# Optimization experiments

Hardware: AMD Instinct MI355X
Metric: run time of the kernel (lower is better)

The kernel has to match this reference:

```python
import jax, jax.numpy as jnp
import numpy as np

B, N, C, H, S = 8, 1024, 768, 8, 16  # C = 3 * S * S, head_dim = C // H
NCH = 3
D = C // H
SCALE = D ** -0.5
REATTEN_SCALE = 1.0  # transform_scale=False
EPS = 1e-5  # BatchNorm2d eps


def conv3x3(x, w, b):
    # x: (B*N, 3, S, S); w: (O=3, I=3, 3, 3) OIHW; 'same' padding
    y = jax.lax.conv_general_dilated(x, w, (1, 1), 'SAME',
                                     dimension_numbers=('NCHW', 'OIHW', 'NCHW'))
    return y + b[None, :, None, None]


def setup_inputs() -> dict:
    key = jax.random.key(0)
    ks = jax.random.split(key, 8)
    return {
        'x': jax.random.normal(ks[0], (B, N, C), jnp.float32),
        'qw': jax.random.normal(ks[1], (NCH, NCH, 3, 3), jnp.float32) * 0.1,
        'qb': jnp.zeros((NCH,), jnp.float32),
        'kw': jax.random.normal(ks[2], (NCH, NCH, 3, 3), jnp.float32) * 0.1,
        'kb': jnp.zeros((NCH,), jnp.float32),
        'vw': jax.random.normal(ks[3], (NCH, NCH, 3, 3), jnp.float32) * 0.1,
        'vb': jnp.zeros((NCH,), jnp.float32),
        'rw': jax.random.normal(ks[4], (H, H), jnp.float32) * 0.2,  # 1x1 conv over heads
        'rb': jnp.zeros((H,), jnp.float32),
        'bn_g': jnp.ones((H,), jnp.float32),
        'bn_b': jnp.zeros((H,), jnp.float32),
        'bn_m': jnp.zeros((H,), jnp.float32),   # running mean
        'bn_v': jnp.ones((H,), jnp.float32),    # running var
        'pw': jax.random.normal(ks[5], (C, C), jnp.float32) * 0.02,
        'pb': jnp.zeros((C,), jnp.float32),
    }


def reference(x, qw, qb, kw, kb, vw, vb, rw, rb, bn_g, bn_b, bn_m, bn_v, pw, pb):
    Bx, Nx, Cx = x.shape
    xs = x.reshape(Bx * Nx, NCH, S, S)  # unflatten; all (b, n) convs batched at once

    def heads(y):  # (B*N, 3, S, S) -> (B, H, N, D)
        return y.reshape(Bx, Nx, H, D).transpose(0, 2, 1, 3)

    q = heads(conv3x3(xs, qw, qb))
    k = heads(conv3x3(xs, kw, kb))
    v = heads(conv3x3(xs, vw, vb))

    attn = jnp.einsum('bhnd,bhmd->bhnm', q, k) * SCALE  # (B, H, N, N)
    attn = jax.nn.softmax(attn, axis=-1)
    # re-attention: 1x1 conv across heads, then BatchNorm2d (eval, running stats)
    attn = jnp.einsum('oh,bhnm->bonm', rw, attn) + rb[None, :, None, None]
    inv = (bn_g / jnp.sqrt(bn_v + EPS))[None, :, None, None]
    attn = (attn - bn_m[None, :, None, None]) * inv + bn_b[None, :, None, None]
    attn = attn * REATTEN_SCALE

    out = jnp.einsum('bhnm,bhmd->bhnd', attn, v)  # (B, H, N, D)
    out = out.transpose(0, 2, 1, 3).reshape(Bx, Nx, Cx)
    out = out @ pw.T + pb
    return (out, attn)
```

## Files before the change

kernel.cpp:

```cpp
#include <hip/hip_runtime.h>
#include <math.h>

#define B_ 8
#define N_ 1024
#define C_ 768
#define H_ 8
#define D_ 96
#define SCALE_F 0.1020620726159657f

typedef unsigned short u16;
typedef __bf16 bf16x8 __attribute__((ext_vector_type(8)));
typedef float f32x4 __attribute__((ext_vector_type(4)));

#define MFMA(a, b, c) __builtin_amdgcn_mfma_f32_16x16x32_bf16(a, b, c, 0, 0, 0)

__device__ inline void split1(float x, u16& h, u16& l) {
    __bf16 hb = (__bf16)x;
    float hf = (float)hb;
    __bf16 lb = (__bf16)(x - hf);
    h = __builtin_bit_cast(u16, hb);
    l = __builtin_bit_cast(u16, lb);
}

__device__ inline void split4(float4 x, ushort4& h, ushort4& l) {
    split1(x.x, h.x, l.x);
    split1(x.y, h.y, l.y);
    split1(x.z, h.z, l.z);
    split1(x.w, h.w, l.w);
}

__global__ __launch_bounds__(256) void conv_qkv(
    const float* __restrict__ x,
    const float* __restrict__ qw, const float* __restrict__ qb,
    const float* __restrict__ kw, const float* __restrict__ kb,
    const float* __restrict__ vw, const float* __restrict__ vb,
    u16* __restrict__ qh, u16* __restrict__ ql,
    u16* __restrict__ kh, u16* __restrict__ kl,
    float* __restrict__ v)
{
    __shared__ float simg[768];
    __shared__ float sw[243];
    __shared__ float sb[9];
    const int img = blockIdx.x;
    const int b = img >> 10;
    const int tid = threadIdx.x;

    for (int i = tid; i < 768; i += 256) simg[i] = x[(size_t)img * 768 + i];
    if (tid < 243) {
        int g = tid / 81, i = tid % 81;
        const float* w = (g == 0) ? qw : (g == 1) ? kw : vw;
        sw[tid] = w[i];
    }
    if (tid < 9) {
        int g = tid / 3, i = tid % 3;
        const float* bb = (g == 0) ? qb : (g == 1) ? kb : vb;
        sb[tid] = bb[i];
    }
    __syncthreads();

    const int n = img & 1023;
    for (int e = tid; e < 2304; e += 256) {
        int g = e / 768, c = e % 768;
        int oc = c >> 8, rem = c & 255, y = rem >> 4, xx = rem & 15;
        float acc = sb[g * 3 + oc];
        const float* wg = &sw[g * 81 + oc * 27];
        #pragma unroll
        for (int ic = 0; ic < 3; ++ic)
            #pragma unroll
            for (int ky = 0; ky < 3; ++ky) {
                int yy = y + ky - 1;
                if (yy < 0 || yy > 15) continue;
                #pragma unroll
                for (int kx = 0; kx < 3; ++kx) {
                    int xp = xx + kx - 1;
                    if (xp < 0 || xp > 15) continue;
                    acc += wg[ic * 9 + ky * 3 + kx] * simg[ic * 256 + yy * 16 + xp];
                }
            }
        int hh = c / 96, d = c % 96;
        size_t o = ((size_t)(b * 8 + hh) * 1024 + n) * 96 + d;
        if (g == 2) {
            v[o] = acc;
        } else {
            u16 hi, lo;
            split1(acc, hi, lo);
            if (g == 0) { qh[o] = hi; ql[o] = lo; }
            else        { kh[o] = hi; kl[o] = lo; }
        }
    }
}

__global__ __launch_bounds__(256) void vt_split(
    const float* __restrict__ v, u16* __restrict__ vt_h)
{
    __shared__ float t32[32][36];
    const int bh = blockIdx.z, n0 = blockIdx.x * 32, d0 = blockIdx.y * 32;
    const int tid = threadIdx.x;
    {
        int nn = tid >> 3, c4 = (tid & 7) * 4;
        float4 x = *(const float4*)&v[((size_t)bh * 1024 + n0 + nn) * 96 + d0 + c4];
        t32[nn][c4] = x.x; t32[nn][c4 + 1] = x.y;
        t32[nn][c4 + 2] = x.z; t32[nn][c4 + 3] = x.w;
    }
    __syncthreads();
    {
        int d = tid >> 3, n4 = (tid & 7) * 4;
        ushort4 h;
        h.x = __builtin_bit_cast(u16, (__bf16)t32[n4][d]);
        h.y = __builtin_bit_cast(u16, (__bf16)t32[n4 + 1][d]);
        h.z = __builtin_bit_cast(u16, (__bf16)t32[n4 + 2][d]);
        h.w = __builtin_bit_cast(u16, (__bf16)t32[n4 + 3][d]);
        size_t o = ((size_t)bh * 96 + d0 + d) * 1024 + n0 + n4;
        *(ushort4*)&vt_h[o] = h;
    }
}

__global__ __launch_bounds__(256) void pw_split(
    const float* __restrict__ pw, u16* __restrict__ pwh, u16* __restrict__ pwl)
{
    int i = blockIdx.x * 256 + threadIdx.x;
    float4 x = *(const float4*)&pw[(size_t)i * 4];
    ushort4 h, l;
    split4(x, h, l);
    *(ushort4*)&pwh[(size_t)i * 4] = h;
    *(ushort4*)&pwl[(size_t)i * 4] = l;
}

__global__ __launch_bounds__(512) void fused_attn(
    const u16* __restrict__ qh, const u16* __restrict__ ql,
    const u16* __restrict__ kh, const u16* __restrict__ kl,
    const u16* __restrict__ vth,
    const float* __restrict__ rw, const float* __restrict__ rb,
    const float* __restrict__ bn_g, const float* __restrict__ bn_b,
    const float* __restrict__ bn_m, const float* __restrict__ bn_v,
    float* __restrict__ attn, u16* __restrict__ o1h, u16* __restrict__ o1l)
{
    __shared__ float p_lds[2][8][32][36];
    __shared__ float s_w2[8][8];
    __shared__ float s_b2[8];

    const int bid = blockIdx.x;
    const int b = bid & 7;
    const int n0 = (bid >> 3) * 32;
    const int tid = threadIdx.x, wid = tid >> 6, lane = tid & 63;
    const int l16 = lane & 15, kg = lane >> 4;
    const int h = wid;
    const size_t bh = (size_t)(b * 8 + h);

    if (tid < 64) {
        int o = tid >> 3, hh = tid & 7;
        float inv = bn_g[o] * rsqrtf(bn_v[o] + 1e-5f);
        s_w2[o][hh] = rw[o * 8 + hh] * inv;
        if (hh == 0) s_b2[o] = (rb[o] - bn_m[o]) * inv + bn_b[o];
    }

    bf16x8 qhf[2][3], qlf[2][3];
    #pragma unroll
    for (int nf = 0; nf < 2; ++nf)
        #pragma unroll
        for (int ks = 0; ks < 3; ++ks) {
            size_t off = (bh * 1024 + n0 + nf * 16 + l16) * 96 + ks * 32 + kg * 8;
            qhf[nf][ks] = *(const bf16x8*)&qh[off];
            qlf[nf][ks] = *(const bf16x8*)&ql[off];
        }

    float ls[2][4];
    #pragma unroll
    for (int nf = 0; nf < 2; ++nf)
        #pragma unroll
        for (int r = 0; r < 4; ++r) ls[nf][r] = 0.f;

    #pragma unroll 1
    for (int mt = 0; mt < 16; ++mt) {
        const int m0 = mt * 64;
        f32x4 sacc[2][4];
        #pragma unroll
        for (int nf = 0; nf < 2; ++nf)
            #pragma unroll
            for (int mf = 0; mf < 4; ++mf) sacc[nf][mf] = (f32x4){0.f, 0.f, 0.f, 0.f};

        __builtin_amdgcn_s_setprio(1);
        #pragma unroll
        for (int ks = 0; ks < 3; ++ks) {
            bf16x8 kbh[4];
            #pragma unroll
            for (int mf = 0; mf < 4; ++mf) {
                size_t off = (bh * 1024 + m0 + mf * 16 + l16) * 96 + ks * 32 + kg * 8;
                kbh[mf] = *(const bf16x8*)&kh[off];
            }
            #pragma unroll
            for (int nf = 0; nf < 2; ++nf)
                #pragma unroll
                for (int mf = 0; mf < 4; ++mf)
                    sacc[nf][mf] = MFMA(qhf[nf][ks], kbh[mf], sacc[nf][mf]);
        }
        __builtin_amdgcn_s_setprio(0);

        #pragma unroll
        for (int nf = 0; nf < 2; ++nf)
            #pragma unroll
            for (int mf = 0; mf < 4; ++mf)
                #pragma unroll
                for (int r = 0; r < 4; ++r)
                    ls[nf][r] += __expf(sacc[nf][mf][r] * SCALE_F);
    }

    float rv[2][4];
    #pragma unroll
    for (int nf = 0; nf < 2; ++nf)
        #pragma unroll
        for (int r = 0; r < 4; ++r) {
            float s = ls[nf][r];
            #pragma unroll
            for (int off = 1; off < 16; off <<= 1) s += __shfl_xor(s, off);
            rv[nf][r] = 1.0f / s;
        }

    __syncthreads();

    float w2r[8];
    #pragma unroll
    for (int hh = 0; hh < 8; ++hh) w2r[hh] = s_w2[h][hh];
    const float b2h = s_b2[h];

    f32x4 pvacc[2][6];
    #pragma unroll
    for (int nf = 0; nf < 2; ++nf)
        #pragma unroll
        for (int df = 0; df < 6; ++df) pvacc[nf][df] = (f32x4){0.f, 0.f, 0.f, 0.f};

    #pragma unroll 1
    for (int mt = 0; mt < 32; ++mt) {
        const int m0 = mt * 32;
        const int buf = mt & 1;

        bf16x8 vbh[6];
        #pragma unroll
        for (int df = 0; df < 6; ++df) {
            size_t off = (bh * 96 + df * 16 + l16) * 1024 + m0 + kg * 8;
            vbh[df] = *(const bf16x8*)&vth[off];
        }

        f32x4 sacc[2][2];
        #pragma unroll
        for (int nf = 0; nf < 2; ++nf)
            #pragma unroll
            for (int mf = 0; mf < 2; ++mf) sacc[nf][mf] = (f32x4){0.f, 0.f, 0.f, 0.f};
        __builtin_amdgcn_s_setprio(1);
        #pragma unroll
        for (int ks = 0; ks < 3; ++ks) {
            bf16x8 kbh[2], kbl[2];
            #pragma unroll
            for (int mf = 0; mf < 2; ++mf) {
                size_t off = (bh * 1024 + m0 + mf * 16 + l16) * 96 + ks * 32 + kg * 8;
                kbh[mf] = *(const bf16x8*)&kh[off];
                kbl[mf] = *(const bf16x8*)&kl[off];
            }
            #pragma unroll
            for (int nf = 0; nf < 2; ++nf)
                #pragma unroll
                for (int mf = 0; mf < 2; ++mf) {
                    sacc[nf][mf] = MFMA(qhf[nf][ks], kbh[mf], sacc[nf][mf]);
                    sacc[nf][mf] = MFMA(qhf[nf][ks], kbl[mf], sacc[nf][mf]);
                    sacc[nf][mf] = MFMA(qlf[nf][ks], kbh[mf], sacc[nf][mf]);
                }
        }
        __builtin_amdgcn_s_setprio(0);

        #pragma unroll
        for (int nf = 0; nf < 2; ++nf)
            #pragma unroll
            for (int mf = 0; mf < 2; ++mf)
                #pragma unroll
                for (int r = 0; r < 4; ++r) {
                    float pp = __expf(sacc[nf][mf][r] * SCALE_F) * rv[nf][r];
                    p_lds[buf][h][nf * 16 + kg * 4 + r][mf * 16 + l16] = pp;
                }
        __syncthreads();

        float mixf[2][8];
        #pragma unroll
        for (int nf = 0; nf < 2; ++nf)
            #pragma unroll
            for (int j = 0; j < 8; ++j) mixf[nf][j] = b2h;
        #pragma unroll
        for (int hh = 0; hh < 8; ++hh) {
            float w = w2r[hh];
            #pragma unroll
            for (int nf = 0; nf < 2; ++nf) {
                const float* pp = &p_lds[buf][hh][nf * 16 + l16][kg * 8];
                float4 a0 = *(const float4*)pp;
                float4 a1 = *(const float4*)(pp + 4);
                mixf[nf][0] += w * a0.x; mixf[nf][1] += w * a0.y;
                mixf[nf][2] += w * a0.z; mixf[nf][3] += w * a0.w;
                mixf[nf][4] += w * a1.x; mixf[nf][5] += w * a1.y;
                mixf[nf][6] += w * a1.z; mixf[nf][7] += w * a1.w;
            }
        }

        #pragma unroll
        for (int nf = 0; nf < 2; ++nf) {
            float* gp = &attn[(bh * 1024 + n0 + nf * 16 + l16) * 1024 + m0 + kg * 8];
            f32x4 v0 = {mixf[nf][0], mixf[nf][1], mixf[nf][2], mixf[nf][3]};
            f32x4 v1 = {mixf[nf][4], mixf[nf][5], mixf[nf][6], mixf[nf][7]};
            __builtin_nontemporal_store(v0, (f32x4*)gp);
            __builtin_nontemporal_store(v1, (f32x4*)(gp + 4));
        }

        bf16x8 mah[2];
        #pragma unroll
        for (int nf = 0; nf < 2; ++nf)
            #pragma unroll
            for (int j = 0; j < 8; ++j)
                mah[nf][j] = (__bf16)mixf[nf][j];
        __builtin_amdgcn_s_setprio(1);
        #pragma unroll
        for (int df = 0; df < 6; ++df)
            #pragma unroll
            for (int nf = 0; nf < 2; ++nf)
                pvacc[nf][df] = MFMA(mah[nf], vbh[df], pvacc[nf][df]);
        __builtin_amdgcn_s_setprio(0);
    }

    #pragma unroll
    for (int nf = 0; nf < 2; ++nf)
        #pragma unroll
        for (int df = 0; df < 6; ++df)
            #pragma unroll
            for (int r = 0; r < 4; ++r) {
                int row = n0 + nf * 16 + kg * 4 + r;
                int col = h * 96 + df * 16 + l16;
                u16 hh2, ll2;
                split1(pvacc[nf][df][r], hh2, ll2);
                size_t o = ((size_t)b * 1024 + row) * 768 + col;
                o1h[o] = hh2;
                o1l[o] = ll2;
            }
}

__global__ __launch_bounds__(256) void proj_mfma(
    const u16* __restrict__ o1h, const u16* __restrict__ o1l,
    const u16* __restrict__ pwh, const u16* __restrict__ pwl,
    const float* __restrict__ pb, float* __restrict__ out)
{
    __shared__ __align__(16) u16 Ahs[5120], Als[5120];
    __shared__ __align__(16) u16 Bhs[2560], Bls[2560];
    const int t0 = blockIdx.y * 128, o0 = blockIdx.x * 64;
    const int tid = threadIdx.x;
    const int wid = tid >> 6, lane = tid & 63;
    const int l16 = lane & 15, kg = lane >> 4;
    const int wr = wid >> 1, wc = wid & 1;

    f32x4 acc[4][2];
    #pragma unroll
    for (int i = 0; i < 4; ++i)
        #pragma unroll
        for (int j = 0; j < 2; ++j) acc[i][j] = (f32x4){0.f, 0.f, 0.f, 0.f};

    for (int s = 0; s < 24; ++s) {
        const int kc = s * 32;
        if (s) __syncthreads();
        #pragma unroll
        for (int i = 0; i < 4; ++i) {
            int idx = tid + i * 256;
            int r = idx >> 3, c4 = idx & 7;
            *(ushort4*)&Ahs[r * 40 + c4 * 4] = *(const ushort4*)&o1h[(size_t)(t0 + r) * 768 + kc + c4 * 4];
            *(ushort4*)&Als[r * 40 + c4 * 4] = *(const ushort4*)&o1l[(size_t)(t0 + r) * 768 + kc + c4 * 4];
        }
        #pragma unroll
        for (int i = 0; i < 2; ++i) {
            int idx = tid + i * 256;
            int r = idx >> 3, c4 = idx & 7;
            *(ushort4*)&Bhs[r * 40 + c4 * 4] = *(const ushort4*)&pwh[(size_t)(o0 + r) * 768 + kc + c4 * 4];
            *(ushort4*)&Bls[r * 40 + c4 * 4] = *(const ushort4*)&pwl[(size_t)(o0 + r) * 768 + kc + c4 * 4];
        }
        __syncthreads();

        bf16x8 ah[4], al[4], bh8[2], bl8[2];
        #pragma unroll
        for (int f = 0; f < 4; ++f) {
            int ra = (wr * 64 + f * 16 + l16) * 40 + kg * 8;
            ah[f] = *(const bf16x8*)&Ahs[ra];
            al[f] = *(const bf16x8*)&Als[ra];
        }
        #pragma unroll
        for (int j = 0; j < 2; ++j) {
            int rb = (wc * 32 + j * 16 + l16) * 40 + kg * 8;
            bh8[j] = *(const bf16x8*)&Bhs[rb];
            bl8[j] = *(const bf16x8*)&Bls[rb];
        }
        #pragma unroll
        for (int i = 0; i < 4; ++i)
            #pragma unroll
            for (int j = 0; j < 2; ++j) {
                acc[i][j] = MFMA(ah[i], bh8[j], acc[i][j]);
                acc[i][j] = MFMA(ah[i], bl8[j], acc[i][j]);
                acc[i][j] = MFMA(al[i], bh8[j], acc[i][j]);
            }
    }

    #pragma unroll
    for (int i = 0; i < 4; ++i) {
        int rr = t0 + wr * 64 + i * 16 + kg * 4;
        #pragma unroll
        for (int j = 0; j < 2; ++j) {
            int cc = o0 + wc * 32 + j * 16 + l16;
            float bias = pb[cc];
            #pragma unroll
            for (int r = 0; r < 4; ++r)
                __builtin_nontemporal_store(acc[i][j][r] + bias,
                                            &out[(size_t)(rr + r) * 768 + cc]);
        }
    }
}

extern "C" void kernel_launch(void* const* d_in, const int* in_sizes, int n_in,
                              void* d_out, int out_size, void* d_ws, size_t ws_size,
                              hipStream_t stream)
{
    const float* x    = (const float*)d_in[0];
    const float* qw   = (const float*)d_in[1];
    const float* qb   = (const float*)d_in[2];
    const float* kw   = (const float*)d_in[3];
    const float* kb   = (const float*)d_in[4];
    const float* vw   = (const float*)d_in[5];
    const float* vb   = (const float*)d_in[6];
    const float* rw   = (const float*)d_in[7];
    const float* rb   = (const float*)d_in[8];
    const float* bn_g = (const float*)d_in[9];
    const float* bn_b = (const float*)d_in[10];
    const float* bn_m = (const float*)d_in[11];
    const float* bn_v = (const float*)d_in[12];
    const float* pw   = (const float*)d_in[13];
    const float* pb   = (const float*)d_in[14];

    float* out_p  = (float*)d_out;
    float* attn_p = out_p + (size_t)B_ * N_ * C_;

    float* ws = (float*)d_ws;
    const size_t qkv = (size_t)B_ * H_ * N_ * D_;

    float* vf  = ws;
    u16* qhp = (u16*)(ws + qkv);
    u16* qlp = qhp + qkv;
    u16* khp = qlp + qkv;
    u16* klp = khp + qkv;
    u16* vth = (u16*)(ws + 3 * qkv);
    u16* o1h = (u16*)(ws + 4 * qkv);
    u16* o1l = o1h + qkv;
    u16* pwh = (u16*)(ws + 5 * qkv);
    u16* pwl = pwh + (size_t)C_ * C_;

    conv_qkv<<<B_ * N_, 256, 0, stream>>>(x, qw, qb, kw, kb, vw, vb,
                                          qhp, qlp, khp, klp, vf);
    vt_split<<<dim3(32, 3, 64), 256, 0, stream>>>(vf, vth);
    pw_split<<<576, 256, 0, stream>>>(pw, pwh, pwl);
    fused_attn<<<256, 512, 0, stream>>>(qhp, qlp, khp, klp, vth,
                                        rw, rb, bn_g, bn_b, bn_m, bn_v,
                                        attn_p, o1h, o1l);
    proj_mfma<<<dim3(12, 64), 256, 0, stream>>>(o1h, o1l, pwh, pwl, pb, out_p);
}
```

Measured before the change: 309.3 us.

## Software-pipeline QK exp for next tile ahead of head-mix and PV

Computes the QK^T scores and softmax numerators for tile mt+1 into the alternate LDS buffer before the head-mixing and PV MFMA work for tile mt. A prologue computes tile 0 first, and a lightweight LDS-wait-plus-barrier sits at the end of each iteration. The goal is to overlap the score MFMAs and exp with the LDS reads and mixing of the previous tile, hiding barrier latency. It raises register pressure because both stages' live values overlap.

```diff
diff --git a/kernel.cpp b/kernel.cpp
--- a/kernel.cpp
+++ b/kernel.cpp
@@ -27,6 +27,11 @@
     split1(x.y, h.y, l.y);
     split1(x.z, h.z, l.z);
     split1(x.w, h.w, l.w);
+}
+
+__device__ inline void bar_lds() {
+    asm volatile("s_waitcnt lgkmcnt(0)" ::: "memory");
+    __builtin_amdgcn_s_barrier();
 }
 
 __global__ __launch_bounds__(256) void conv_qkv(
@@ -229,6 +234,49 @@
         #pragma unroll
         for (int df = 0; df < 6; ++df) pvacc[nf][df] = (f32x4){0.f, 0.f, 0.f, 0.f};
 
+#define QKEXP(MT, BUF)                                                          \
+    {                                                                           \
+        const int m0_ = (MT) * 32;                                              \
+        f32x4 sacc_[2][2];                                                      \
+        _Pragma("unroll")                                                       \
+        for (int nf_ = 0; nf_ < 2; ++nf_)                                       \
+            _Pragma("unroll")                                                   \
+            for (int mf_ = 0; mf_ < 2; ++mf_)                                   \
+                sacc_[nf_][mf_] = (f32x4){0.f, 0.f, 0.f, 0.f};                  \
+        __builtin_amdgcn_s_setprio(1);                                          \
+        _Pragma("unroll")                                                       \
+        for (int ks_ = 0; ks_ < 3; ++ks_) {                                     \
+            bf16x8 kbh_[2], kbl_[2];                                            \
+            _Pragma("unroll")                                                   \
+            for (int mf_ = 0; mf_ < 2; ++mf_) {                                 \
+                size_t off_ = (bh * 1024 + m0_ + mf_ * 16 + l16) * 96 + ks_ * 32 + kg * 8; \
+                kbh_[mf_] = *(const bf16x8*)&kh[off_];                          \
+                kbl_[mf_] = *(const bf16x8*)&kl[off_];                          \
+            }                                                                   \
+            _Pragma("unroll")                                                   \
+            for (int nf_ = 0; nf_ < 2; ++nf_)                                   \
+                _Pragma("unroll")                                               \
+                for (int mf_ = 0; mf_ < 2; ++mf_) {                             \
+                    sacc_[nf_][mf_] = MFMA(qhf[nf_][ks_], kbh_[mf_], sacc_[nf_][mf_]); \
+                    sacc_[nf_][mf_] = MFMA(qhf[nf_][ks_], kbl_[mf_], sacc_[nf_][mf_]); \
+                    sacc_[nf_][mf_] = MFMA(qlf[nf_][ks_], kbh_[mf_], sacc_[nf_][mf_]); \
+                }                                                               \
+        }                                                                       \
+        __builtin_amdgcn_s_setprio(0);                                          \
+        _Pragma("unroll")                                                       \
+        for (int nf_ = 0; nf_ < 2; ++nf_)                                       \
+            _Pragma("unroll")                                                   \
+            for (int mf_ = 0; mf_ < 2; ++mf_)                                   \
+                _Pragma("unroll")                                               \
+                for (int r_ = 0; r_ < 4; ++r_) {                                \
+                    float pp_ = __expf(sacc_[nf_][mf_][r_] * SCALE_F) * rv[nf_][r_]; \
+                    p_lds[BUF][h][nf_ * 16 + kg * 4 + r_][mf_ * 16 + l16] = pp_; \
+                }                                                               \
+    }
+
+    QKEXP(0, 0)
+    bar_lds();
+
     #pragma unroll 1
     for (int mt = 0; mt < 32; ++mt) {
         const int m0 = mt * 32;
@@ -241,42 +289,7 @@
             vbh[df] = *(const bf16x8*)&vth[off];
         }
 
-        f32x4 sacc[2][2];
-        #pragma unroll
-        for (int nf = 0; nf < 2; ++nf)
-            #pragma unroll
-            for (int mf = 0; mf < 2; ++mf) sacc[nf][mf] = (f32x4){0.f, 0.f, 0.f, 0.f};
-        __builtin_amdgcn_s_setprio(1);
-        #pragma unroll
-        for (int ks = 0; ks < 3; ++ks) {
-            bf16x8 kbh[2], kbl[2];
-            #pragma unroll
-            for (int mf = 0; mf < 2; ++mf) {
-                size_t off = (bh * 1024 + m0 + mf * 16 + l16) * 96 + ks * 32 + kg * 8;
-                kbh[mf] = *(const bf16x8*)&kh[off];
-                kbl[mf] = *(const bf16x8*)&kl[off];
-            }
-            #pragma unroll
-            for (int nf = 0; nf < 2; ++nf)
-                #pragma unroll
-                for (int mf = 0; mf < 2; ++mf) {
-                    sacc[nf][mf] = MFMA(qhf[nf][ks], kbh[mf], sacc[nf][mf]);
-                    sacc[nf][mf] = MFMA(qhf[nf][ks], kbl[mf], sacc[nf][mf]);
-                    sacc[nf][mf] = MFMA(qlf[nf][ks], kbh[mf], sacc[nf][mf]);
-                }
-        }
-        __builtin_amdgcn_s_setprio(0);
-
-        #pragma unroll
-        for (int nf = 0; nf < 2; ++nf)
-            #pragma unroll
-            for (int mf = 0; mf < 2; ++mf)
-                #pragma unroll
-                for (int r = 0; r < 4; ++r) {
-                    float pp = __expf(sacc[nf][mf][r] * SCALE_F) * rv[nf][r];
-                    p_lds[buf][h][nf * 16 + kg * 4 + r][mf * 16 + l16] = pp;
-                }
-        __syncthreads();
+        if (mt < 31) QKEXP(mt + 1, buf ^ 1)
 
         float mixf[2][8];
         #pragma unroll
@@ -320,7 +333,10 @@
             for (int nf = 0; nf < 2; ++nf)
                 pvacc[nf][df] = MFMA(mah[nf], vbh[df], pvacc[nf][df]);
         __builtin_amdgcn_s_setprio(0);
-    }
+
+        bar_lds();
+    }
+#undef QKEXP
 
     #pragma unroll
     for (int nf = 0; nf < 2; ++nf)
```

After: 294.6 us. 4.7% less time.
